# Kernel tuning notes

Hardware: AMD Instinct MI355X
Metric: run time of the kernel (lower is better)

The kernel has to match this reference:

```python
import jax, jax.numpy as jnp
import numpy as np

B, H, N = 512, 128, 32      # batch, horizon, lidar sectors
D = 75                      # state dim (32 sectors + 32 diff + 11 non-lidar)
NON_AUG = 17                # 11 non-lidar + 6 aux stats
SM = 32                     # sector_model_dim
HALF = 128                  # embed_dim // 2
EMB = 256                   # embed_dim
DYAW_IDX = 72               # 64 + 3 + 2 + 2 + 1
NO_ECHO = 0.95


def linear(x, W, b):
    # torch nn.Linear: y = x @ W.T + b, W: (out, in)
    return jnp.einsum('...i,oi->...o', x, W) + b


def layernorm(x, w, b, eps=1e-5):
    m = x.mean(-1, keepdims=True)
    v = ((x - m) ** 2).mean(-1, keepdims=True)
    return (x - m) / jnp.sqrt(v + eps) * w + b


def setup_inputs() -> dict:
    key = jax.random.key(0)
    ks = jax.random.split(key, 10)
    f32 = jnp.float32
    return {
        'state_seq': jax.random.uniform(ks[0], (B, H, D), dtype=f32),
        'token_W': jax.random.normal(ks[1], (SM, 3), dtype=f32) * 0.3,
        'token_b': jnp.zeros((SM,), f32),
        'query_W': jax.random.normal(ks[2], (SM, NON_AUG), dtype=f32) * 0.2,
        'query_b': jnp.zeros((SM,), f32),
        'range_bias_scale': jnp.asarray(1.0, f32),
        'valid_bias': jnp.asarray(0.0, f32),
        'invalid_bias': jnp.asarray(-1.0, f32),
        'att_ln_w': jnp.ones((SM,), f32),
        'att_ln_b': jnp.zeros((SM,), f32),
        'non_W': jax.random.normal(ks[3], (HALF, NON_AUG), dtype=f32) * 0.2,
        'non_b': jnp.zeros((HALF,), f32),
        'spfb_W': jax.random.normal(ks[4], (HALF, 3), dtype=f32) * 0.3,
        'spfb_b': jnp.zeros((HALF,), f32),
        'sp_gate': jnp.asarray(-4.0, f32),
        'spatial_W': jax.random.normal(ks[5], (HALF, SM), dtype=f32) * 0.15,
        'spatial_b': jnp.zeros((HALF,), f32),
        'fuse_W': jax.random.normal(ks[6], (EMB, 2 * HALF), dtype=f32) * 0.06,
        'fuse_b': jnp.zeros((EMB,), f32),
        'ln_w': jnp.ones((EMB,), f32),
        'ln_b': jnp.zeros((EMB,), f32),
    }


def _forward(state_seq, token_W, token_b, query_W, query_b,
             range_bias_scale, valid_bias, invalid_bias, att_ln_w, att_ln_b,
             non_W, non_b, spfb_W, spfb_b, sp_gate,
             spatial_W, spatial_b, fuse_W, fuse_b, ln_w, ln_b):
    sectors = state_seq[:, :, 0:N]            # (B,H,N)
    lidar_diff = state_seq[:, :, N:2 * N]     # (B,H,N)
    non_lidar = state_seq[:, :, 2 * N:D]      # (B,H,11)

    valid = (sectors < NO_ECHO).astype(state_seq.dtype)
    min_r = sectors.min(axis=-1)
    mean_r = sectors.mean(axis=-1)
    valid_ratio = valid.mean(axis=-1)
    diff_abs = jnp.abs(lidar_diff)
    diff_abs_mean = diff_abs.mean(axis=-1)
    diff_abs_max = diff_abs.max(axis=-1)
    dyaw_abs = jnp.clip(jnp.abs(state_seq[:, :, DYAW_IDX]), 0.0, 1.0)
    diff_mag = jnp.clip(diff_abs_mean, 0.0, 1.0)

    aux = jnp.stack([min_r, mean_r, valid_ratio, diff_abs_mean, diff_abs_max, dyaw_abs], axis=-1)
    non_aug = jnp.concatenate([non_lidar, aux], axis=-1)  # (B,H,17)
    non_emb = jax.nn.relu(linear(non_aug, non_W, non_b))  # (B,H,HALF)

    sp_fallback = jnp.stack([min_r, mean_r, valid_ratio], axis=-1)
    sp_fallback_emb = jax.nn.relu(linear(sp_fallback, spfb_W, spfb_b))

    # --- spatial sector attention ---
    tok = jnp.stack([sectors, lidar_diff, valid], axis=-1)        # (B,H,N,3)
    tok_emb = jax.nn.relu(linear(tok, token_W, token_b))          # (B,H,N,SM)
    q = jax.nn.relu(linear(non_aug, query_W, query_b))[:, :, None, :]  # (B,H,1,SM)
    score = (tok_emb * q).sum(axis=-1) / np.sqrt(SM)              # (B,H,N)
    score = score + range_bias_scale * (1.0 - sectors)
    score = score + valid_bias * valid + invalid_bias * (1.0 - valid)
    w = jax.nn.softmax(score, axis=-1)
    ctx = (w[..., None] * tok_emb).sum(axis=2)                    # (B,H,SM)
    ctx = layernorm(ctx, att_ln_w, att_ln_b)

    sp_att_emb = jax.nn.relu(linear(ctx, spatial_W, spatial_b))
    alpha = jax.nn.sigmoid(sp_gate)
    sp_emb = alpha * sp_att_emb + (1.0 - alpha) * sp_fallback_emb

    x = jnp.concatenate([non_emb, sp_emb], axis=-1)
    x = jax.nn.relu(linear(x, fuse_W, fuse_b))
    x = layernorm(x, ln_w, ln_b)
    time_feats = jnp.stack([diff_mag, dyaw_abs], axis=-1)
    return x, time_feats


def reference(state_seq, token_W, token_b, query_W, query_b,
              range_bias_scale, valid_bias, invalid_bias, att_ln_w, att_ln_b,
              non_W, non_b, spfb_W, spfb_b, sp_gate,
              spatial_W, spatial_b, fuse_W, fuse_b, ln_w, ln_b):
    return _forward(state_seq, token_W, token_b, query_W, query_b,
                    range_bias_scale, valid_bias, invalid_bias, att_ln_w, att_ln_b,
                    non_W, non_b, spfb_W, spfb_b, sp_gate,
                    spatial_W, spatial_b, fuse_W, fuse_b, ln_w, ln_b)
```

## Files before the change

### kernel.cpp

```cpp
#include <hip/hip_runtime.h>

#define BH      65536
#define DSTATE  75
#define EMBD    256
#define NROWS   32
#define NTHREADS 512
#define NBLOCKS (BH / NROWS)

typedef _Float16 h2    __attribute__((ext_vector_type(2)));
typedef _Float16 f16x8 __attribute__((ext_vector_type(8)));
typedef float    f32x4 __attribute__((ext_vector_type(4)));

__device__ __forceinline__ h2 u2h(unsigned int u) {
    union { unsigned int u; h2 h; } c; c.u = u; return c.h;
}
__device__ __forceinline__ unsigned int h2u(h2 h) {
    union { h2 h; unsigned int u; } c; c.h = h; return c.u;
}
__device__ __forceinline__ unsigned int packh2(float a, float b) {
    union { h2 h; unsigned int u; } c;
    c.h = h2{(_Float16)a, (_Float16)b}; return c.u;
}
__device__ __forceinline__ h2 pkrtz(float a, float b) {
#if __has_builtin(__builtin_amdgcn_cvt_pkrtz)
    auto r = __builtin_amdgcn_cvt_pkrtz(a, b);
    return *reinterpret_cast<h2*>(&r);
#else
    return h2{(_Float16)a, (_Float16)b};
#endif
}
__device__ __forceinline__ float fdot2(h2 a, h2 b, float c) {
#if __has_builtin(__builtin_amdgcn_fdot2)
    return __builtin_amdgcn_fdot2(a, b, c, false);
#else
    return c + (float)a[0] * (float)b[0] + (float)a[1] * (float)b[1];
#endif
}
__device__ __forceinline__ h2 pkfma(h2 a, h2 b, h2 c) {
#if __has_builtin(__builtin_elementwise_fma)
    return __builtin_elementwise_fma(a, b, c);
#else
    return a * b + c;
#endif
}

template<int CTRL>
__device__ __forceinline__ float dppmv(float x) {
    return __builtin_bit_cast(float,
        __builtin_amdgcn_update_dpp(0, __builtin_bit_cast(int, x), CTRL, 0xF, 0xF, true));
}
template<int IMM>
__device__ __forceinline__ float swz(float x) {
    return __builtin_bit_cast(float,
        __builtin_amdgcn_ds_swizzle(__builtin_bit_cast(int, x), IMM));
}
#define ROR1 0x121
#define ROR2 0x122
#define ROR4 0x124
#define ROR8 0x128
#define QXOR1 0xB1
#define SWZ_XOR16 0x401F
#define SWZ_BC8   0x0100

__device__ __forceinline__ float sum32(float x) {
    x += dppmv<ROR1>(x); x += dppmv<ROR2>(x);
    x += dppmv<ROR4>(x); x += dppmv<ROR8>(x);
    return x + swz<SWZ_XOR16>(x);
}
__device__ __forceinline__ float sum16(float x) {
    x += dppmv<ROR1>(x); x += dppmv<ROR2>(x);
    x += dppmv<ROR4>(x); x += dppmv<ROR8>(x);
    return x;
}

__global__ __launch_bounds__(256) void prep_w_kernel(
    const float* __restrict__ fuse_W, const float* __restrict__ non_W,
    const float* __restrict__ spatial_W, const float* __restrict__ query_W,
    const float* __restrict__ token_W, const float* __restrict__ token_b,
    unsigned short* __restrict__ ws)
{
    int id = blockIdx.x * 256 + threadIdx.x;
    if (id < 8192) {
        int wl = id & 63, ct = (id >> 6) & 15, ks = id >> 10;
        int n = ct * 16 + (wl & 15);
        int k0 = ks * 32 + (wl >> 4) * 8;
        const float* src = fuse_W + n * 256 + k0;
        float4 a = *reinterpret_cast<const float4*>(src);
        float4 b = *reinterpret_cast<const float4*>(src + 4);
        uint4 o = make_uint4(packh2(a.x, a.y), packh2(a.z, a.w),
                             packh2(b.x, b.y), packh2(b.z, b.w));
        reinterpret_cast<uint4*>(ws)[id] = o;
    } else if (id < 8704) {
        int i = id - 8192;
        int wl = i & 63, ct = i >> 6;
        int n = ct * 16 + (wl & 15);
        int k0 = (wl >> 4) * 8;
        float v[8];
        #pragma unroll
        for (int j = 0; j < 8; ++j) {
            int k = k0 + j;
            v[j] = (k < 17) ? non_W[n * 17 + k] : 0.0f;
        }
        uint4 o = make_uint4(packh2(v[0], v[1]), packh2(v[2], v[3]),
                             packh2(v[4], v[5]), packh2(v[6], v[7]));
        reinterpret_cast<uint4*>(ws)[8192 + i] = o;
    } else if (id < 9216) {
        int i = id - 8704;
        int wl = i & 63, ct = i >> 6;
        int n = ct * 16 + (wl & 15);
        int k0 = (wl >> 4) * 8;
        const float* src = spatial_W + n * 32 + k0;
        float4 a = *reinterpret_cast<const float4*>(src);
        float4 b = *reinterpret_cast<const float4*>(src + 4);
        uint4 o = make_uint4(packh2(a.x, a.y), packh2(a.z, a.w),
                             packh2(b.x, b.y), packh2(b.z, b.w));
        reinterpret_cast<uint4*>(ws)[8704 + i] = o;
    } else if (id < 9728) {
        int i = id - 9216;
        int feat = i >> 4, j = i & 15;
        int k0 = 2 * j, k1 = 2 * j + 1;
        float a = (k0 < 17) ? query_W[feat * 17 + k0] : 0.0f;
        float b = (k1 < 17) ? query_W[feat * 17 + k1] : 0.0f;
        unsigned int* qWh = reinterpret_cast<unsigned int*>(ws + 73728);
        qWh[i] = packh2(a, b);
    } else if (id < 9856) {
        int i = id - 9728;
        int tbl = i >> 5, k = i & 31;
        float v = (tbl < 3) ? token_W[3 * k + tbl] : token_b[k];
        unsigned int* TWb = reinterpret_cast<unsigned int*>(ws + 73728) + 512;
        TWb[i] = packh2(v, v);
    } else if (id < 9920) {
        int i = id - 9856;
        int tbl = i >> 4, j = i & 15;
        int k0 = 2 * j, k1 = 2 * j + 1;
        float a = (tbl < 3) ? token_W[3 * k0 + tbl] : token_b[k0];
        float b = (tbl < 3) ? token_W[3 * k1 + tbl] : token_b[k1];
        unsigned int* TWp = reinterpret_cast<unsigned int*>(ws + 73728) + 640;
        TWp[i] = packh2(a, b);
    }
}

__global__ __launch_bounds__(512, 8) void att_state_enc_kernel(
    const float* __restrict__ state,
    const float* __restrict__ query_b,
    const float* __restrict__ rbs_p, const float* __restrict__ vb_p, const float* __restrict__ ivb_p,
    const float* __restrict__ att_ln_w, const float* __restrict__ att_ln_b,
    const float* __restrict__ non_b,
    const float* __restrict__ spfb_W, const float* __restrict__ spfb_b,
    const float* __restrict__ sp_gate_p,
    const float* __restrict__ spatial_b,
    const unsigned short* __restrict__ Wf, const unsigned short* __restrict__ Wn,
    const unsigned short* __restrict__ Ws,
    const unsigned int* __restrict__ qWh, const unsigned int* __restrict__ TWb,
    const unsigned int* __restrict__ TWp,
    const float* __restrict__ fuse_b,
    const float* __restrict__ ln_w, const float* __restrict__ ln_b,
    float* __restrict__ out_x, float* __restrict__ out_tf)
{
    __shared__ __align__(16) float4 s_fb4[NROWS];
    __shared__ __align__(16) _Float16 s_na_h[NROWS][40];
    __shared__ __align__(16) _Float16 s_ctx_h[NROWS][40];
    __shared__ __align__(16) unsigned int s_q2[NROWS][16];
    __shared__ __align__(16) uint4 s_p4[NROWS][16];
    __shared__ __align__(16) _Float16 s_x[NROWS][280];
    __shared__ __align__(16) float2 s_part[NROWS][4];
    __shared__ __align__(16) float2 s_mr[NROWS];
    __shared__ float  s_tf[NROWS * 2];

    const int t = threadIdx.x;
    const int g = t >> 5;
    const int l = t & 31;
    const long rowbase = (long)blockIdx.x * NROWS;

    const float rbs = rbs_p[0];
    const float vb  = vb_p[0];
    const float ivb = ivb_p[0];
    const float qb = query_b[l];
    const uint4* qwp = reinterpret_cast<const uint4*>(qWh + l * 16);
    const uint4 qw0 = qwp[0], qw1 = qwp[1], qw2 = qwp[2];
    const h2 zero2 = h2{(_Float16)0.0f, (_Float16)0.0f};
    const unsigned long long halfmask =
        0xFFFFFFFFull << (((unsigned)t & 32u));

    #pragma unroll
    for (int rr = 0; rr < 2; ++rr) {
        const int row = g + 16 * rr;
        const long gb = (rowbase + row) * DSTATE;

        float sec = state[gb + l];
        float dif = state[gb + 32 + l];
        float nl  = (l < 11) ? state[gb + 64 + l] : 0.0f;
        float vld = (sec < 0.95f) ? 1.0f : 0.0f;
        float da  = fabsf(dif);
        float vs = (float)__popcll(__ballot(sec < 0.95f) & halfmask);
        float mn = sec, sm = sec, ds = da, dmx = da;
        {
            mn = fminf(mn, dppmv<ROR1>(mn)); sm += dppmv<ROR1>(sm);
            ds += dppmv<ROR1>(ds); dmx = fmaxf(dmx, dppmv<ROR1>(dmx));
            mn = fminf(mn, dppmv<ROR2>(mn)); sm += dppmv<ROR2>(sm);
            ds += dppmv<ROR2>(ds); dmx = fmaxf(dmx, dppmv<ROR2>(dmx));
            mn = fminf(mn, dppmv<ROR4>(mn)); sm += dppmv<ROR4>(sm);
            ds += dppmv<ROR4>(ds); dmx = fmaxf(dmx, dppmv<ROR4>(dmx));
            mn = fminf(mn, dppmv<ROR8>(mn)); sm += dppmv<ROR8>(sm);
            ds += dppmv<ROR8>(ds); dmx = fmaxf(dmx, dppmv<ROR8>(dmx));
            mn = fminf(mn, swz<SWZ_XOR16>(mn)); sm += swz<SWZ_XOR16>(sm);
            ds += swz<SWZ_XOR16>(ds);
            dmx = fmaxf(dmx, swz<SWZ_XOR16>(dmx));
        }
        const float min_r = mn, mean_r = sm * (1.0f/32.0f), vr = vs * (1.0f/32.0f);
        const float dam = ds * (1.0f/32.0f), dax = dmx;
        const float dyaw = fminf(fabsf(swz<SWZ_BC8>(nl)), 1.0f);

        float naval = 0.0f;
        if (l < 11)       naval = nl;
        else if (l == 11) naval = min_r;
        else if (l == 12) naval = mean_r;
        else if (l == 13) naval = vr;
        else if (l == 14) naval = dam;
        else if (l == 15) naval = dax;
        else if (l == 16) naval = dyaw;
        s_na_h[row][l] = (_Float16)naval;
        if (l == 0) {
            s_fb4[row] = make_float4(min_r, mean_r, vr, 0.0f);
            s_tf[row * 2] = fminf(dam, 1.0f); s_tf[row * 2 + 1] = dyaw;
        }

        {
            const uint4* nap = reinterpret_cast<const uint4*>(&s_na_h[row][0]);
            uint4 n0 = nap[0], n1 = nap[1], n2 = nap[2];
            float a0 = qb, a1 = 0.0f;
            a0 = fdot2(u2h(qw0.x), u2h(n0.x), a0);
            a1 = fdot2(u2h(qw0.y), u2h(n0.y), a1);
            a0 = fdot2(u2h(qw0.z), u2h(n0.z), a0);
            a1 = fdot2(u2h(qw0.w), u2h(n0.w), a1);
            a0 = fdot2(u2h(qw1.x), u2h(n1.x), a0);
            a1 = fdot2(u2h(qw1.y), u2h(n1.y), a1);
            a0 = fdot2(u2h(qw1.z), u2h(n1.z), a0);
            a1 = fdot2(u2h(qw1.w), u2h(n1.w), a1);
            a0 = fdot2(u2h(qw2.x), u2h(n2.x), a0);
            float qv = fmaxf(a0 + a1, 0.0f);
            float qn = dppmv<QXOR1>(qv);
            if ((l & 1) == 0) s_q2[row][l >> 1] = h2u(pkrtz(qv, qn));
        }

        {
            unsigned int q2[16];
            *reinterpret_cast<uint4*>(&q2[0])  = *reinterpret_cast<const uint4*>(&s_q2[row][0]);
            *reinterpret_cast<uint4*>(&q2[4])  = *reinterpret_cast<const uint4*>(&s_q2[row][4]);
            *reinterpret_cast<uint4*>(&q2[8])  = *reinterpret_cast<const uint4*>(&s_q2[row][8]);
            *reinterpret_cast<uint4*>(&q2[12]) = *reinterpret_cast<const uint4*>(&s_q2[row][12]);
            const h2 sec2 = pkrtz(sec, sec);
            const h2 dif2 = pkrtz(dif, dif);
            const h2 vld2 = pkrtz(vld, vld);
            float a0 = 0.0f, a1 = 0.0f;
            #pragma unroll
            for (int j = 0; j < 16; j += 2) {
                h2 z0 = pkfma(vld2, u2h(TWp[32 + j]), u2h(TWp[48 + j]));
                z0 = pkfma(dif2, u2h(TWp[16 + j]), z0);
                z0 = pkfma(sec2, u2h(TWp[j]), z0);
                z0 = __builtin_elementwise_max(z0, zero2);
                a0 = fdot2(z0, u2h(q2[j]), a0);
                h2 z1 = pkfma(vld2, u2h(TWp[33 + j]), u2h(TWp[49 + j]));
                z1 = pkfma(dif2, u2h(TWp[17 + j]), z1);
                z1 = pkfma(sec2, u2h(TWp[1 + j]), z1);
                z1 = __builtin_elementwise_max(z1, zero2);
                a1 = fdot2(z1, u2h(q2[j + 1]), a1);
            }
            float score = (a0 + a1) * 0.17677669529663687f
                        + rbs * (1.0f - sec) + vb * vld + ivb * (1.0f - vld);
            score = fminf(fmaxf(score, -60.0f), 60.0f);
            float e = __expf(score - 20.0f);
            float se = sum32(e);
            float w = __fdividef(e, se);
            float wn = dppmv<QXOR1>(w);
            float sn = dppmv<QXOR1>(sec);
            float dn = dppmv<QXOR1>(dif);
            float vn = dppmv<QXOR1>(vld);
            if ((l & 1) == 0) {
                uint4 pk = make_uint4(h2u(pkrtz(w, wn)), h2u(pkrtz(sec, sn)),
                                      h2u(pkrtz(dif, dn)), h2u(pkrtz(vld, vn)));
                s_p4[row][l >> 1] = pk;
            }
        }

        {
            const h2 tw0b = u2h(TWb[l]);
            const h2 tw1b = u2h(TWb[32 + l]);
            const h2 tw2b = u2h(TWb[64 + l]);
            const h2 tbb  = u2h(TWb[96 + l]);
            float a0 = 0.0f, a1 = 0.0f;
            #pragma unroll
            for (int i = 0; i < 16; i += 2) {
                uint4 p0 = s_p4[row][i];
                h2 z0 = pkfma(u2h(p0.w), tw2b, tbb);
                z0 = pkfma(u2h(p0.z), tw1b, z0);
                z0 = pkfma(u2h(p0.y), tw0b, z0);
                z0 = __builtin_elementwise_max(z0, zero2);
                a0 = fdot2(u2h(p0.x), z0, a0);
                uint4 p1 = s_p4[row][i + 1];
                h2 z1 = pkfma(u2h(p1.w), tw2b, tbb);
                z1 = pkfma(u2h(p1.z), tw1b, z1);
                z1 = pkfma(u2h(p1.y), tw0b, z1);
                z1 = __builtin_elementwise_max(z1, zero2);
                a1 = fdot2(u2h(p1.x), z1, a1);
            }
            float acc = a0 + a1;
            float smv = acc, sq = acc * acc;
            smv += dppmv<ROR1>(smv); sq += dppmv<ROR1>(sq);
            smv += dppmv<ROR2>(smv); sq += dppmv<ROR2>(sq);
            smv += dppmv<ROR4>(smv); sq += dppmv<ROR4>(sq);
            smv += dppmv<ROR8>(smv); sq += dppmv<ROR8>(sq);
            smv += swz<SWZ_XOR16>(smv); sq += swz<SWZ_XOR16>(sq);
            float mean = smv * (1.0f/32.0f);
            float var  = sq * (1.0f/32.0f) - mean * mean;
            float rstd = rsqrtf(var + 1e-5f);
            float ctx = (acc - mean) * rstd * att_ln_w[l] + att_ln_b[l];
            s_ctx_h[row][l] = (_Float16)ctx;
        }
    }
    __syncthreads();

    const int wid = t >> 6, wl = t & 63;
    const int arow = wl & 15, kg = wl >> 4;
    const int m = wid & 1, cq = wid >> 1;

    {
        if (t < NROWS * 2) out_tf[rowbase * 2 + t] = s_tf[t];

        const float alpha = 1.0f / (1.0f + __expf(-sp_gate_p[0]));
        const int rbase = m * 16;
        f16x8 a_na  = *reinterpret_cast<const f16x8*>(&s_na_h[rbase + arow][kg * 8]);
        f16x8 a_ctx = *reinterpret_cast<const f16x8*>(&s_ctx_h[rbase + arow][kg * 8]);
        float mnr[4], mer[4], vrr[4];
        #pragma unroll
        for (int r = 0; r < 4; ++r) {
            float4 fb4 = s_fb4[rbase + kg * 4 + r];
            mnr[r] = fb4.x; mer[r] = fb4.y; vrr[r] = fb4.z;
        }
        #pragma unroll
        for (int tt = 0; tt < 2; ++tt) {
            const int ct = cq + tt * 4;
            const int col = ct * 16 + arow;
            f16x8 bN = *reinterpret_cast<const f16x8*>(Wn + ((ct * 64) + wl) * 8);
            f16x8 bS = *reinterpret_cast<const f16x8*>(Ws + ((ct * 64) + wl) * 8);
            f32x4 accN = __builtin_amdgcn_mfma_f32_16x16x32_f16(a_na,  bN, f32x4{0.f,0.f,0.f,0.f}, 0,0,0);
            f32x4 accS = __builtin_amdgcn_mfma_f32_16x16x32_f16(a_ctx, bS, f32x4{0.f,0.f,0.f,0.f}, 0,0,0);
            const float nb = non_b[col], sb = spatial_b[col];
            const float w0 = spfb_W[col*3], w1 = spfb_W[col*3+1], w2 = spfb_W[col*3+2];
            const float fbb = spfb_b[col];
            #pragma unroll
            for (int r = 0; r < 4; ++r) {
                const int row = rbase + kg * 4 + r;
                float ne = fmaxf(accN[r] + nb, 0.0f);
                float sa = fmaxf(accS[r] + sb, 0.0f);
                float fb = fmaxf(fbb + w0*mnr[r] + w1*mer[r] + w2*vrr[r], 0.0f);
                float sp = alpha * sa + (1.0f - alpha) * fb;
                float nen = dppmv<QXOR1>(ne);
                float spn = dppmv<QXOR1>(sp);
                if ((arow & 1) == 0) {
                    *reinterpret_cast<unsigned int*>(&s_x[row][col])       = h2u(pkrtz(ne, nen));
                    *reinterpret_cast<unsigned int*>(&s_x[row][128 + col]) = h2u(pkrtz(sp, spn));
                }
            }
        }
    }
    __syncthreads();

    float v[4][4];
    {
        f32x4 acc[4];
        #pragma unroll
        for (int i = 0; i < 4; ++i) acc[i] = f32x4{0.f, 0.f, 0.f, 0.f};
        #pragma unroll
        for (int ks = 0; ks < 8; ++ks) {
            f16x8 a = *reinterpret_cast<const f16x8*>(&s_x[m * 16 + arow][ks * 32 + kg * 8]);
            #pragma unroll
            for (int i = 0; i < 4; ++i) {
                const int ct = cq * 4 + i;
                f16x8 b = *reinterpret_cast<const f16x8*>(Wf + (((ks * 16 + ct) * 64) + wl) * 8);
                acc[i] = __builtin_amdgcn_mfma_f32_16x16x32_f16(a, b, acc[i], 0, 0, 0);
            }
        }
        float psum[4] = {0.f, 0.f, 0.f, 0.f};
        float psq[4]  = {0.f, 0.f, 0.f, 0.f};
        #pragma unroll
        for (int i = 0; i < 4; ++i) {
            const int col = (cq * 4 + i) * 16 + arow;
            const float bias = fuse_b[col];
            #pragma unroll
            for (int r = 0; r < 4; ++r) {
                float x = fmaxf(acc[i][r] + bias, 0.0f);
                v[i][r] = x;
                psum[r] += x;
                psq[r]  += x * x;
            }
        }
        #pragma unroll
        for (int r = 0; r < 4; ++r) {
            psum[r] = sum16(psum[r]);
            psq[r]  = sum16(psq[r]);
        }
        if (arow == 0) {
            #pragma unroll
            for (int r = 0; r < 4; ++r)
                s_part[m * 16 + kg * 4 + r][cq] = make_float2(psum[r], psq[r]);
        }
    }
    __syncthreads();

    if (t < NROWS) {
        const float4* pp = reinterpret_cast<const float4*>(&s_part[t][0]);
        float4 pa = pp[0], pb = pp[1];
        float sum = pa.x + pa.z + pb.x + pb.z;
        float sq  = pa.y + pa.w + pb.y + pb.w;
        float mean = sum * (1.0f/256.0f);
        float var  = sq * (1.0f/256.0f) - mean * mean;
        float rstd = rsqrtf(var + 1e-5f);
        s_mr[t] = make_float2(mean, rstd);
    }
    __syncthreads();

    {
        float lwv[4], lbv[4];
        #pragma unroll
        for (int i = 0; i < 4; ++i) {
            const int col = (cq * 4 + i) * 16 + arow;
            lwv[i] = ln_w[col]; lbv[i] = ln_b[col];
        }
        #pragma unroll
        for (int r = 0; r < 4; ++r) {
            const int row = m * 16 + kg * 4 + r;
            float2 mr = s_mr[row];
            const long obase = (rowbase + row) * EMBD;
            #pragma unroll
            for (int i = 0; i < 4; ++i) {
                const int col = (cq * 4 + i) * 16 + arow;
                out_x[obase + col] = (v[i][r] - mr.x) * mr.y * lwv[i] + lbv[i];
            }
        }
    }
}

extern "C" void kernel_launch(void* const* d_in, const int* in_sizes, int n_in,
                              void* d_out, int out_size, void* d_ws, size_t ws_size,
                              hipStream_t stream) {
    const float* state     = (const float*)d_in[0];
    const float* token_W   = (const float*)d_in[1];
    const float* token_b   = (const float*)d_in[2];
    const float* query_W   = (const float*)d_in[3];
    const float* query_b   = (const float*)d_in[4];
    const float* rbs       = (const float*)d_in[5];
    const float* vbias     = (const float*)d_in[6];
    const float* ivbias    = (const float*)d_in[7];
    const float* att_ln_w  = (const float*)d_in[8];
    const float* att_ln_b  = (const float*)d_in[9];
    const float* non_W     = (const float*)d_in[10];
    const float* non_b     = (const float*)d_in[11];
    const float* spfb_W    = (const float*)d_in[12];
    const float* spfb_b    = (const float*)d_in[13];
    const float* sp_gate   = (const float*)d_in[14];
    const float* spatial_W = (const float*)d_in[15];
    const float* spatial_b = (const float*)d_in[16];
    const float* fuse_W    = (const float*)d_in[17];
    const float* fuse_b    = (const float*)d_in[18];
    const float* ln_w      = (const float*)d_in[19];
    const float* ln_b      = (const float*)d_in[20];

    float* out_x  = (float*)d_out;
    float* out_tf = out_x + (size_t)BH * EMBD;

    unsigned short* wsu = (unsigned short*)d_ws;
    const unsigned short* Wf = wsu;
    const unsigned short* Wn = wsu + 65536;
    const unsigned short* Ws = wsu + 65536 + 4096;
    const unsigned int* qWh = (const unsigned int*)(wsu + 73728);
    const unsigned int* TWb = qWh + 512;
    const unsigned int* TWp = TWb + 128;

    hipLaunchKernelGGL(prep_w_kernel, dim3(39), dim3(256), 0, stream,
                       fuse_W, non_W, spatial_W, query_W, token_W, token_b, wsu);

    hipLaunchKernelGGL(att_state_enc_kernel, dim3(NBLOCKS), dim3(NTHREADS), 0, stream,
        state, query_b, rbs, vbias, ivbias,
        att_ln_w, att_ln_b, non_b, spfb_W, spfb_b, sp_gate, spatial_b,
        Wf, Wn, Ws, qWh, TWb, TWp, fuse_b, ln_w, ln_b, out_x, out_tf);
}
```

Baseline: 54.00 us.

## Halve block size to 256 threads with each wave covering more rows and columns

Cuts the block from 512 to 256 threads while keeping 32 rows per block. Each warp now handles four input rows instead of two, and each MFMA wave covers 4 or 8 column tiles instead of 2 or 4. The LayerNorm partial-sum array shrinks from four to two entries per row. This is meant to amortise per-thread setup and weight loads over more work and reduce cross-wave reductions, at the cost of more registers per thread (a v[8][4] accumulator) and fewer threads available to hide latency.

```diff
diff --git a/kernel.cpp b/kernel.cpp
--- a/kernel.cpp
+++ b/kernel.cpp
@@ -4,7 +4,7 @@
 #define DSTATE  75
 #define EMBD    256
 #define NROWS   32
-#define NTHREADS 512
+#define NTHREADS 256
 #define NBLOCKS (BH / NROWS)
 
 typedef _Float16 h2    __attribute__((ext_vector_type(2)));
@@ -140,7 +140,7 @@
     }
 }
 
-__global__ __launch_bounds__(512, 8) void att_state_enc_kernel(
+__global__ __launch_bounds__(256, 4) void att_state_enc_kernel(
     const float* __restrict__ state,
     const float* __restrict__ query_b,
     const float* __restrict__ rbs_p, const float* __restrict__ vb_p, const float* __restrict__ ivb_p,
@@ -163,7 +163,7 @@
     __shared__ __align__(16) unsigned int s_q2[NROWS][16];
     __shared__ __align__(16) uint4 s_p4[NROWS][16];
     __shared__ __align__(16) _Float16 s_x[NROWS][280];
-    __shared__ __align__(16) float2 s_part[NROWS][4];
+    __shared__ __align__(16) float2 s_part[NROWS][2];
     __shared__ __align__(16) float2 s_mr[NROWS];
     __shared__ float  s_tf[NROWS * 2];
 
@@ -183,8 +183,8 @@
         0xFFFFFFFFull << (((unsigned)t & 32u));
 
     #pragma unroll
-    for (int rr = 0; rr < 2; ++rr) {
-        const int row = g + 16 * rr;
+    for (int rr = 0; rr < 4; ++rr) {
+        const int row = g + 8 * rr;
         const long gb = (rowbase + row) * DSTATE;
 
         float sec = state[gb + l];
@@ -322,13 +322,13 @@
 
     const int wid = t >> 6, wl = t & 63;
     const int arow = wl & 15, kg = wl >> 4;
-    const int m = wid & 1, cq = wid >> 1;
+    const int m = wid & 1, cqb = wid >> 1;
+    const int rbase = m * 16;
 
     {
         if (t < NROWS * 2) out_tf[rowbase * 2 + t] = s_tf[t];
 
         const float alpha = 1.0f / (1.0f + __expf(-sp_gate_p[0]));
-        const int rbase = m * 16;
         f16x8 a_na  = *reinterpret_cast<const f16x8*>(&s_na_h[rbase + arow][kg * 8]);
         f16x8 a_ctx = *reinterpret_cast<const f16x8*>(&s_ctx_h[rbase + arow][kg * 8]);
         float mnr[4], mer[4], vrr[4];
@@ -338,8 +338,8 @@
             mnr[r] = fb4.x; mer[r] = fb4.y; vrr[r] = fb4.z;
         }
         #pragma unroll
-        for (int tt = 0; tt < 2; ++tt) {
-            const int ct = cq + tt * 4;
+        for (int tt = 0; tt < 4; ++tt) {
+            const int ct = cqb * 4 + tt;
             const int col = ct * 16 + arow;
             f16x8 bN = *reinterpret_cast<const f16x8*>(Wn + ((ct * 64) + wl) * 8);
             f16x8 bS = *reinterpret_cast<const f16x8*>(Ws + ((ct * 64) + wl) * 8);
@@ -366,17 +366,17 @@
     }
     __syncthreads();
 
-    float v[4][4];
+    float v[8][4];
     {
-        f32x4 acc[4];
-        #pragma unroll
-        for (int i = 0; i < 4; ++i) acc[i] = f32x4{0.f, 0.f, 0.f, 0.f};
+        f32x4 acc[8];
+        #pragma unroll
+        for (int i = 0; i < 8; ++i) acc[i] = f32x4{0.f, 0.f, 0.f, 0.f};
         #pragma unroll
         for (int ks = 0; ks < 8; ++ks) {
-            f16x8 a = *reinterpret_cast<const f16x8*>(&s_x[m * 16 + arow][ks * 32 + kg * 8]);
-            #pragma unroll
-            for (int i = 0; i < 4; ++i) {
-                const int ct = cq * 4 + i;
+            f16x8 a = *reinterpret_cast<const f16x8*>(&s_x[rbase + arow][ks * 32 + kg * 8]);
+            #pragma unroll
+            for (int i = 0; i < 8; ++i) {
+                const int ct = cqb * 8 + i;
                 f16x8 b = *reinterpret_cast<const f16x8*>(Wf + (((ks * 16 + ct) * 64) + wl) * 8);
                 acc[i] = __builtin_amdgcn_mfma_f32_16x16x32_f16(a, b, acc[i], 0, 0, 0);
             }
@@ -384,8 +384,8 @@
         float psum[4] = {0.f, 0.f, 0.f, 0.f};
         float psq[4]  = {0.f, 0.f, 0.f, 0.f};
         #pragma unroll
-        for (int i = 0; i < 4; ++i) {
-            const int col = (cq * 4 + i) * 16 + arow;
+        for (int i = 0; i < 8; ++i) {
+            const int col = (cqb * 8 + i) * 16 + arow;
             const float bias = fuse_b[col];
             #pragma unroll
             for (int r = 0; r < 4; ++r) {
@@ -403,16 +403,15 @@
         if (arow == 0) {
             #pragma unroll
             for (int r = 0; r < 4; ++r)
-                s_part[m * 16 + kg * 4 + r][cq] = make_float2(psum[r], psq[r]);
+                s_part[rbase + kg * 4 + r][cqb] = make_float2(psum[r], psq[r]);
         }
     }
     __syncthreads();
 
     if (t < NROWS) {
-        const float4* pp = reinterpret_cast<const float4*>(&s_part[t][0]);
-        float4 pa = pp[0], pb = pp[1];
-        float sum = pa.x + pa.z + pb.x + pb.z;
-        float sq  = pa.y + pa.w + pb.y + pb.w;
+        float4 pa = *reinterpret_cast<const float4*>(&s_part[t][0]);
+        float sum = pa.x + pa.z;
+        float sq  = pa.y + pa.w;
         float mean = sum * (1.0f/256.0f);
         float var  = sq * (1.0f/256.0f) - mean * mean;
         float rstd = rsqrtf(var + 1e-5f);
@@ -421,21 +420,15 @@
     __syncthreads();
 
     {
-        float lwv[4], lbv[4];
-        #pragma unroll
-        for (int i = 0; i < 4; ++i) {
-            const int col = (cq * 4 + i) * 16 + arow;
-            lwv[i] = ln_w[col]; lbv[i] = ln_b[col];
-        }
         #pragma unroll
         for (int r = 0; r < 4; ++r) {
-            const int row = m * 16 + kg * 4 + r;
+            const int row = rbase + kg * 4 + r;
             float2 mr = s_mr[row];
             const long obase = (rowbase + row) * EMBD;
             #pragma unroll
-            for (int i = 0; i < 4; ++i) {
-                const int col = (cq * 4 + i) * 16 + arow;
-                out_x[obase + col] = (v[i][r] - mr.x) * mr.y * lwv[i] + lbv[i];
+            for (int i = 0; i < 8; ++i) {
+                const int col = (cqb * 8 + i) * 16 + arow;
+                out_x[obase + col] = (v[i][r] - mr.x) * mr.y * ln_w[col] + ln_b[col];
             }
         }
     }
```

New measurement: 54.94 us. About the same (+1.7%).
